# Kernel optimization log

Measured on AMD Instinct MI355X. Metric: run time of the kernel, lower is better.

Reference implementation:

```python
import jax, jax.numpy as jnp
import numpy as np

N_NODES = 100000
N_EDGES = 1600000
IN_CH = 128
HEADS = 4
OUT_CH = 32


def setup_inputs() -> dict:
    key = jax.random.key(0)
    k1, k2, k3, k4 = jax.random.split(key, 4)
    x = jax.random.normal(k1, (N_NODES, IN_CH), dtype=jnp.float32)
    edge_index = jax.random.randint(k2, (2, N_EDGES), 0, N_NODES, dtype=jnp.int64)
    # linear weight stored as [in, heads*out] so projection is x @ W
    W = jax.random.normal(k3, (IN_CH, HEADS * OUT_CH), dtype=jnp.float32) * (1.0 / np.sqrt(IN_CH))
    att = jax.random.normal(k4, (HEADS, OUT_CH), dtype=jnp.float32)
    return {"x": x, "edge_index": edge_index, "W": W, "att": att}


def reference(x, edge_index, W, att):
    N = x.shape[0]
    row, col = edge_index[0], edge_index[1]
    # project and split heads: [N, H, C]
    projected = (x @ W).reshape(N, HEADS, OUT_CH)
    src = projected[row]                      # [E, H, C]
    dst = projected[col]                      # [E, H, C]
    scores = jnp.tanh(src + dst)              # [E, H, C]
    scores = jnp.einsum('ehc,hc->eh', scores, att)  # [E, H]
    # stabilize by global per-head max over edges, then exp
    scores = jnp.exp(scores - jnp.max(scores, axis=0, keepdims=True))
    # scatter-add over destination nodes
    out = jax.ops.segment_sum(src * scores[:, :, None], col, num_segments=N)  # [N, H, C]
    normalizer = jax.ops.segment_sum(scores, col, num_segments=N)             # [N, H]
    out = out / jnp.maximum(normalizer, 1e-12)[:, :, None]
    return out.reshape(N, HEADS * OUT_CH)
```

## Files before the change

kernel.cpp:

```cpp
#include <hip/hip_runtime.h>

#define IN_CH 128
#define HEADS 4
#define OUT_CH 32
#define HC 128
#define SCORE_BLOCKS 4096
#define CHUNK 2048

__device__ __forceinline__ unsigned flip_f32(float x) {
  unsigned u = __float_as_uint(x);
  return (u & 0x80000000u) ? ~u : (u | 0x80000000u);
}
__device__ __forceinline__ float unflip_f32(unsigned k) {
  unsigned u = (k & 0x80000000u) ? (k ^ 0x80000000u) : ~k;
  return __uint_as_float(u);
}
__device__ __forceinline__ float fast_tanh(float x) {
#if __has_builtin(__builtin_amdgcn_exp2f)
  const float t = __builtin_amdgcn_exp2f(x * 2.8853900817779268f);
#else
  const float t = __expf(2.f * x);
#endif
#if __has_builtin(__builtin_amdgcn_rcpf)
  return 1.f - 2.f * __builtin_amdgcn_rcpf(t + 1.f);
#else
  return 1.f - 2.f / (t + 1.f);
#endif
}

__global__ __launch_bounds__(256) void gemm_xW(const float* __restrict__ x,
                                               const float* __restrict__ W,
                                               float* __restrict__ proj, int N,
                                               const int* __restrict__ ecol,
                                               int* __restrict__ hist, int E) {
  __shared__ float xs[128][68];
  __shared__ float ws[128][68];
  const int tid = threadIdx.x;
  const int rowblk = blockIdx.x >> 1;
  const int colblk = blockIdx.x & 1;
  const int row0 = rowblk * 64;
  const int col0 = colblk * 64;

  {
    const int k = tid >> 1;
    const int c0 = (tid & 1) * 32;
    const float4* src = (const float4*)(W + (size_t)k * HC + col0 + c0);
#pragma unroll
    for (int i = 0; i < 8; ++i) *(float4*)&ws[k][c0 + i * 4] = src[i];
  }
  {
    const int r = tid >> 2;
    const int k0 = (tid & 3) * 32;
    const int grow = row0 + r;
    const bool valid = grow < N;
    const float4* src = (const float4*)(x + (size_t)grow * IN_CH + k0);
#pragma unroll
    for (int i = 0; i < 8; ++i) {
      float4 v = valid ? src[i] : make_float4(0.f, 0.f, 0.f, 0.f);
      const int k = k0 + i * 4;
      xs[k][r] = v.x; xs[k + 1][r] = v.y; xs[k + 2][r] = v.z; xs[k + 3][r] = v.w;
    }
  }
  __syncthreads();

  const int cg2 = tid & 15;
  const int rg = tid >> 4;
  float acc[4][4];
#pragma unroll
  for (int r = 0; r < 4; ++r)
#pragma unroll
    for (int c = 0; c < 4; ++c) acc[r][c] = 0.f;

#pragma unroll 8
  for (int k = 0; k < 128; ++k) {
    const float4 a = *(const float4*)&xs[k][rg * 4];
    const float4 b = *(const float4*)&ws[k][cg2 * 4];
    const float xv[4] = {a.x, a.y, a.z, a.w};
    const float wv[4] = {b.x, b.y, b.z, b.w};
#pragma unroll
    for (int r = 0; r < 4; ++r)
#pragma unroll
      for (int c = 0; c < 4; ++c) acc[r][c] += xv[r] * wv[c];
  }

#pragma unroll
  for (int r = 0; r < 4; ++r) {
    const int grow = row0 + rg * 4 + r;
    if (grow < N) {
      *(float4*)(proj + (size_t)grow * HC + col0 + cg2 * 4) =
          make_float4(acc[r][0], acc[r][1], acc[r][2], acc[r][3]);
    }
  }

  if (hist) {
    const int ehb = (E + gridDim.x - 1) / gridDim.x;
    const int estart = blockIdx.x * ehb;
    const int eend = min(estart + ehb, E);
    for (int e = estart + tid; e < eend; e += 256) atomicAdd(&hist[ecol[e]], 1);
  }
}

__device__ __forceinline__ int block_scan_excl(int tsum, int* ls, int tid, int* total) {
  ls[tid] = tsum;
  __syncthreads();
  for (int off = 1; off < 256; off <<= 1) {
    int v = (tid >= off) ? ls[tid - off] : 0;
    __syncthreads();
    ls[tid] += v;
    __syncthreads();
  }
  *total = ls[255];
  return ls[tid] - tsum;
}

__global__ __launch_bounds__(256) void k_scan(const int* __restrict__ hist,
                                              int* __restrict__ sums,
                                              unsigned* __restrict__ flags,
                                              int* __restrict__ starts,
                                              int* __restrict__ cursor,
                                              int nb, int nc) {
  __shared__ int ls[256];
  const int tid = threadIdx.x;
  const int bid = blockIdx.x;
  const int base = bid * CHUNK + tid * 8;
  int h[8];
  int t = 0;
#pragma unroll
  for (int j = 0; j < 8; ++j) {
    const int i = base + j;
    h[j] = (i < nb) ? hist[i] : 0;
    t += h[j];
  }
  int total;
  const int excl = block_scan_excl(t, ls, tid, &total);
  if (tid == 0) {
    __hip_atomic_store(&sums[bid], total, __ATOMIC_RELAXED, __HIP_MEMORY_SCOPE_AGENT);
    __hip_atomic_store(&flags[bid], 1u, __ATOMIC_RELEASE, __HIP_MEMORY_SCOPE_AGENT);
  }
  int my = 0;
  if (tid < bid) {
    while (__hip_atomic_load(&flags[tid], __ATOMIC_ACQUIRE, __HIP_MEMORY_SCOPE_AGENT) == 0u) {}
    my = __hip_atomic_load(&sums[tid], __ATOMIC_RELAXED, __HIP_MEMORY_SCOPE_AGENT);
  }
  __syncthreads();
  ls[tid] = my;
  __syncthreads();
  for (int off = 128; off >= 1; off >>= 1) {
    if (tid < off) ls[tid] += ls[tid + off];
    __syncthreads();
  }
  const int cbase = ls[0];
  int run = cbase + excl;
#pragma unroll
  for (int j = 0; j < 8; ++j) {
    const int i = base + j;
    if (i < nb) { starts[i] = run; cursor[i] = run; run += h[j]; }
  }
  if (bid == nc - 1 && tid == 0) {
    starts[nb] = cbase + total;
    cursor[nb] = cbase + total;
  }
}

__global__ __launch_bounds__(256) void scatter_rc(const int* __restrict__ erow,
                                                  const int* __restrict__ ecol,
                                                  int* __restrict__ cursor,
                                                  int* __restrict__ rc, int E) {
  const int i = blockIdx.x * 256 + threadIdx.x;
  if (i < E) {
    const int p = atomicAdd(&cursor[ecol[i]], 1);
    rc[p] = erow[i] * HC;
  }
}

__global__ __launch_bounds__(256) void fused_apply(const float* __restrict__ proj,
                                                   const int* __restrict__ rc,
                                                   const int* __restrict__ starts,
                                                   const float* __restrict__ att,
                                                   float* __restrict__ out,
                                                   float* __restrict__ den,
                                                   unsigned* __restrict__ headmax_u, int N) {
  __shared__ unsigned blkmax[HEADS];
  const int tid = threadIdx.x;
  if (tid < HEADS) blkmax[tid] = 0u;
  __syncthreads();
  const int lane = tid & 63;
  const int half = lane >> 5;
  const int l = lane & 31;
  const int c0 = l * 4;
  const int head = l >> 3;
  const int n = blockIdx.x * 4 + (tid >> 6);
  float lm = -3.0e38f;

  if (n < N) {
    const float4 a4 = ((const float4*)att)[l];
    float M0 = fabsf(a4.x) + fabsf(a4.y) + fabsf(a4.z) + fabsf(a4.w);
    M0 += __shfl_xor(M0, 4, 64);
    M0 += __shfl_xor(M0, 2, 64);
    M0 += __shfl_xor(M0, 1, 64);
    const float4 d4 = *(const float4*)(proj + (size_t)n * HC + c0);
    const int beg = __builtin_amdgcn_readfirstlane(starts[n]);
    const int end = __builtin_amdgcn_readfirstlane(starts[n + 1]);

    float ax = 0.f, ay = 0.f, az = 0.f, aw = 0.f, dsum = 0.f;
    int i = beg;
    for (; i + 8 <= end; i += 8) {
      const int r0 = rc[i + half];
      const int r1 = rc[i + 2 + half];
      const int r2 = rc[i + 4 + half];
      const int r3 = rc[i + 6 + half];
      const float4 s0 = *(const float4*)(proj + r0 + c0);
      const float4 s1 = *(const float4*)(proj + r1 + c0);
      const float4 s2 = *(const float4*)(proj + r2 + c0);
      const float4 s3 = *(const float4*)(proj + r3 + c0);
      float p0 = fast_tanh(s0.x + d4.x) * a4.x + fast_tanh(s0.y + d4.y) * a4.y
               + fast_tanh(s0.z + d4.z) * a4.z + fast_tanh(s0.w + d4.w) * a4.w;
      float p1 = fast_tanh(s1.x + d4.x) * a4.x + fast_tanh(s1.y + d4.y) * a4.y
               + fast_tanh(s1.z + d4.z) * a4.z + fast_tanh(s1.w + d4.w) * a4.w;
      float p2 = fast_tanh(s2.x + d4.x) * a4.x + fast_tanh(s2.y + d4.y) * a4.y
               + fast_tanh(s2.z + d4.z) * a4.z + fast_tanh(s2.w + d4.w) * a4.w;
      float p3 = fast_tanh(s3.x + d4.x) * a4.x + fast_tanh(s3.y + d4.y) * a4.y
               + fast_tanh(s3.z + d4.z) * a4.z + fast_tanh(s3.w + d4.w) * a4.w;
      p0 += __shfl_xor(p0, 4, 64);  p1 += __shfl_xor(p1, 4, 64);
      p2 += __shfl_xor(p2, 4, 64);  p3 += __shfl_xor(p3, 4, 64);
      p0 += __shfl_xor(p0, 2, 64);  p1 += __shfl_xor(p1, 2, 64);
      p2 += __shfl_xor(p2, 2, 64);  p3 += __shfl_xor(p3, 2, 64);
      p0 += __shfl_xor(p0, 1, 64);  p1 += __shfl_xor(p1, 1, 64);
      p2 += __shfl_xor(p2, 1, 64);  p3 += __shfl_xor(p3, 1, 64);
      lm = fmaxf(lm, fmaxf(fmaxf(p0, p1), fmaxf(p2, p3)));
      const float e0 = __expf(p0 - M0);
      const float e1 = __expf(p1 - M0);
      const float e2 = __expf(p2 - M0);
      const float e3 = __expf(p3 - M0);
      ax += s0.x * e0 + s1.x * e1 + s2.x * e2 + s3.x * e3;
      ay += s0.y * e0 + s1.y * e1 + s2.y * e2 + s3.y * e3;
      az += s0.z * e0 + s1.z * e1 + s2.z * e2 + s3.z * e3;
      aw += s0.w * e0 + s1.w * e1 + s2.w * e2 + s3.w * e3;
      dsum += (e0 + e1) + (e2 + e3);
    }
    if (i + 4 <= end) {
      const int r0 = rc[i + half];
      const int r1 = rc[i + 2 + half];
      const float4 s0 = *(const float4*)(proj + r0 + c0);
      const float4 s1 = *(const float4*)(proj + r1 + c0);
      float p0 = fast_tanh(s0.x + d4.x) * a4.x + fast_tanh(s0.y + d4.y) * a4.y
               + fast_tanh(s0.z + d4.z) * a4.z + fast_tanh(s0.w + d4.w) * a4.w;
      float p1 = fast_tanh(s1.x + d4.x) * a4.x + fast_tanh(s1.y + d4.y) * a4.y
               + fast_tanh(s1.z + d4.z) * a4.z + fast_tanh(s1.w + d4.w) * a4.w;
      p0 += __shfl_xor(p0, 4, 64);  p1 += __shfl_xor(p1, 4, 64);
      p0 += __shfl_xor(p0, 2, 64);  p1 += __shfl_xor(p1, 2, 64);
      p0 += __shfl_xor(p0, 1, 64);  p1 += __shfl_xor(p1, 1, 64);
      lm = fmaxf(lm, fmaxf(p0, p1));
      const float e0 = __expf(p0 - M0);
      const float e1 = __expf(p1 - M0);
      ax += s0.x * e0 + s1.x * e1;
      ay += s0.y * e0 + s1.y * e1;
      az += s0.z * e0 + s1.z * e1;
      aw += s0.w * e0 + s1.w * e1;
      dsum += e0 + e1;
      i += 4;
    }
    for (; i < end; i += 2) {
      const int idx = i + half;
      const bool valid = idx < end;
      const int row = rc[valid ? idx : i];
      const float4 s4 = *(const float4*)(proj + row + c0);
      float p = fast_tanh(s4.x + d4.x) * a4.x
              + fast_tanh(s4.y + d4.y) * a4.y
              + fast_tanh(s4.z + d4.z) * a4.z
              + fast_tanh(s4.w + d4.w) * a4.w;
      p += __shfl_xor(p, 4, 64);
      p += __shfl_xor(p, 2, 64);
      p += __shfl_xor(p, 1, 64);
      if (!valid) p = -3.0e38f;
      lm = fmaxf(lm, p);
      const float e = __expf(p - M0);
      ax += s4.x * e; ay += s4.y * e; az += s4.z * e; aw += s4.w * e;
      dsum += e;
    }
    dsum += __shfl_xor(dsum, 32, 64);
    ax += __shfl_xor(ax, 32, 64);
    ay += __shfl_xor(ay, 32, 64);
    az += __shfl_xor(az, 32, 64);
    aw += __shfl_xor(aw, 32, 64);
    lm = fmaxf(lm, __shfl_xor(lm, 32, 64));
    if (half == 0) {
      const float inv = 1.f / fmaxf(dsum, 1e-38f);
      *(float4*)(out + (size_t)n * HC + c0) =
          make_float4(ax * inv, ay * inv, az * inv, aw * inv);
      if ((l & 7) == 0) den[n * HEADS + head] = dsum;
      if ((l & 7) == 0) atomicMax(&blkmax[head], flip_f32(lm));
    }
  }
  __syncthreads();
  if (tid < HEADS) {
    const unsigned v = blkmax[tid];
    if (v > headmax_u[tid]) atomicMax(&headmax_u[tid], v);
  }
}

__global__ __launch_bounds__(256) void fix_clamp(float* __restrict__ out,
                                                 const float* __restrict__ den,
                                                 const unsigned* __restrict__ headmax_u,
                                                 const float* __restrict__ att, int N) {
  const int t = blockIdx.x * 256 + threadIdx.x;
  if (t >= N * HEADS) return;
  const int n = t >> 2;
  const int h = t & 3;
  float M0 = 0.f;
#pragma unroll
  for (int c = 0; c < OUT_CH; ++c) M0 += fabsf(att[h * OUT_CH + c]);
  const float Mt = unflip_f32(headmax_u[h]);
  const float f = den[t] * __expf(M0 - Mt);
  if (f < 1e-12f) {
    const float s = f * 1e12f;
    float4* p = (float4*)(out + (size_t)n * HC + h * OUT_CH);
#pragma unroll
    for (int j = 0; j < 8; ++j) {
      float4 v = p[j];
      v.x *= s; v.y *= s; v.z *= s; v.w *= s;
      p[j] = v;
    }
  }
}

__global__ __launch_bounds__(256) void reduce_corr(const unsigned* __restrict__ blockmax,
                                                   const float* __restrict__ att,
                                                   float* __restrict__ corr, int nblk) {
  __shared__ unsigned sm[HEADS];
  const int tid = threadIdx.x;
  if (tid < HEADS) sm[tid] = 0u;
  __syncthreads();
  const int h = tid & 3;
  unsigned k = 0u;
  for (int i = tid >> 2; i < nblk; i += 64) k = max(k, blockmax[i * HEADS + h]);
  atomicMax(&sm[h], k);
  __syncthreads();
  if (tid < HEADS) {
    const float Mt = unflip_f32(sm[tid]);
    float M0 = 0.f;
#pragma unroll
    for (int c = 0; c < OUT_CH; ++c) M0 += fabsf(att[tid * OUT_CH + c]);
    corr[tid] = __expf(M0 - Mt);
    corr[4 + tid] = Mt;
  }
}

__global__ __launch_bounds__(256) void score_max(const float* __restrict__ proj,
                                                 const int* __restrict__ erow,
                                                 const int* __restrict__ ecol,
                                                 const float* __restrict__ att,
                                                 unsigned* __restrict__ blockmax, int E) {
  __shared__ unsigned blkmax[HEADS];
  const int tid = threadIdx.x;
  if (tid < HEADS) blkmax[tid] = 0u;
  __syncthreads();
  const int lane = tid & 63;
  const int wid = tid >> 6;
  const float a0 = att[lane];
  const float a1 = att[lane + 64];
  float lmA = -3.0e38f, lmB = -3.0e38f;
  const int stride = SCORE_BLOCKS * 16;

  for (int base = (blockIdx.x * 4 + wid) * 4; base < E; base += stride) {
    const int bu = __builtin_amdgcn_readfirstlane(base);
    const int lim = min(bu + 4, E);
    for (int e = bu; e < lim; ++e) {
      const int r0 = erow[e], c0 = ecol[e];
      const float* ps = proj + (size_t)r0 * HC;
      const float* pd = proj + (size_t)c0 * HC;
      float pA = fast_tanh(ps[lane] + pd[lane]) * a0;
      float pB = fast_tanh(ps[lane + 64] + pd[lane + 64]) * a1;
#pragma unroll
      for (int m = 16; m >= 1; m >>= 1) {
        pA += __shfl_xor(pA, m, 64);
        pB += __shfl_xor(pB, m, 64);
      }
      lmA = fmaxf(lmA, pA);
      lmB = fmaxf(lmB, pB);
    }
  }
  if ((lane & 31) == 0) {
    const int hh = lane >> 5;
    atomicMax(&blkmax[hh], flip_f32(lmA));
    atomicMax(&blkmax[hh + 2], flip_f32(lmB));
  }
  __syncthreads();
  if (tid < HEADS) blockmax[blockIdx.x * HEADS + tid] = blkmax[tid];
}

__global__ __launch_bounds__(256) void edge_apply_fb(const float* __restrict__ proj,
                                                     const int* __restrict__ erow,
                                                     const int* __restrict__ ecol,
                                                     const float* __restrict__ att,
                                                     const float* __restrict__ headmax,
                                                     float* __restrict__ out,
                                                     float* __restrict__ norm, int E) {
  const int tid = threadIdx.x;
  const int e = blockIdx.x * 2 + (tid >> 7);
  if (e >= E) return;
  const int ch = tid & 127;
  const int h = ch >> 5;
  const float M = headmax[h];
  const int row = erow[e];
  const int col = ecol[e];
  const float sv = proj[(size_t)row * HC + ch];
  const float dv = proj[(size_t)col * HC + ch];
  float p = fast_tanh(sv + dv) * att[ch];
#pragma unroll
  for (int m = 16; m >= 1; m >>= 1) p += __shfl_xor(p, m, 64);
  const float w = __expf(p - M);
  unsafeAtomicAdd(&out[(size_t)col * HC + ch], sv * w);
  if ((ch & 31) == 0) unsafeAtomicAdd(&norm[(size_t)col * HEADS + h], w);
}

__global__ __launch_bounds__(256) void finalize_fb(float* __restrict__ out,
                                                   const float* __restrict__ norm, int N) {
  const int idx = blockIdx.x * blockDim.x + threadIdx.x;
  const int total = N * (HC / 4);
  if (idx >= total) return;
  const int base = idx * 4;
  const int node = base >> 7;
  const int h = (base >> 5) & 3;
  const float inv = 1.f / fmaxf(norm[node * HEADS + h], 1e-12f);
  float4 v = ((float4*)out)[idx];
  v.x *= inv; v.y *= inv; v.z *= inv; v.w *= inv;
  ((float4*)out)[idx] = v;
}

extern "C" void kernel_launch(void* const* d_in, const int* in_sizes, int n_in,
                              void* d_out, int out_size, void* d_ws, size_t ws_size,
                              hipStream_t stream) {
  const float* x    = (const float*)d_in[0];
  const int*   eidx = (const int*)d_in[1];
  const float* W    = (const float*)d_in[2];
  const float* att  = (const float*)d_in[3];
  float* out = (float*)d_out;

  const int N = in_sizes[0] / IN_CH;
  const int E = in_sizes[1] / 2;
  const int nb = N;
  const int nc = (nb + CHUNK - 1) / CHUNK;
  const int ngemm = ((N + 63) / 64) * 2;

  char* p = (char*)d_ws;
  float* proj = (float*)p;  p += (size_t)N * HC * 4;
  int* rc = (int*)p;        p += (((size_t)E * 4 + 15) & ~15ull);
  float* den = (float*)p;   p += (((size_t)N * HEADS * 4 + 15) & ~15ull);
  int* hist = (int*)p;      p += (((size_t)(nb + 4 + 256) * 4 + 15) & ~15ull);
  int* starts = (int*)p;    p += (((size_t)(nb + 1) * 4 + 15) & ~15ull);
  int* cursor = (int*)p;    p += (((size_t)(nb + 1) * 4 + 15) & ~15ull);
  int* sums = (int*)p;      p += 1024;
  unsigned* headmax_u = (unsigned*)(hist + nb);
  unsigned* flags = (unsigned*)(hist + nb + 4);
  const size_t need_full = (size_t)(p - (char*)d_ws);
  const bool full = (ws_size >= need_full) && (nc <= 256);

  if (full) {
    hipMemsetAsync(hist, 0, (size_t)(nb + 4 + 256) * sizeof(int), stream);
    gemm_xW<<<ngemm, 256, 0, stream>>>(x, W, proj, N, eidx + E, hist, E);
    k_scan<<<nc, 256, 0, stream>>>(hist, sums, flags, starts, cursor, nb, nc);
    scatter_rc<<<(E + 255) / 256, 256, 0, stream>>>(eidx, eidx + E, cursor, rc, E);
    fused_apply<<<(N + 3) / 4, 256, 0, stream>>>(proj, rc, starts, att, out, den,
                                                 headmax_u, N);
    fix_clamp<<<(N * HEADS + 255) / 256, 256, 0, stream>>>(out, den, headmax_u, att, N);
  } else {
    gemm_xW<<<ngemm, 256, 0, stream>>>(x, W, proj, N, nullptr, nullptr, 0);
    unsigned* bm = (unsigned*)(proj + (size_t)N * HC);
    float* cr = (float*)(bm + SCORE_BLOCKS * HEADS);
    float* norm = cr + 8;
    hipMemsetAsync(out, 0, (size_t)out_size * sizeof(float), stream);
    hipMemsetAsync(norm, 0, (size_t)N * HEADS * sizeof(float), stream);
    score_max<<<SCORE_BLOCKS, 256, 0, stream>>>(proj, eidx, eidx + E, att, bm, E);
    reduce_corr<<<1, 256, 0, stream>>>(bm, att, cr, SCORE_BLOCKS);
    edge_apply_fb<<<(E + 1) / 2, 256, 0, stream>>>(proj, eidx, eidx + E, att, cr + 4, out, norm, E);
    finalize_fb<<<(N * (HC / 4) + 255) / 256, 256, 0, stream>>>(out, norm, N);
  }
}
```

Baseline: 454.0 us.

## Replace global-atomic CSR scatter with two-pass bucketed counting sort

Swaps the single scatter kernel, which did one global atomicAdd per edge on a per-node cursor and wrote to random positions, for a two-pass bucket sort. The first pass groups edges into buckets of 512 destination nodes using shared-memory atomics and one global atomic per bucket per block. The second pass places each bucket's edges into CSR order with shared-memory atomics, so global writes stay local. This adds an 8-byte-per-edge intermediate buffer and an extra kernel launch, and rc order within a node is still non-deterministic.

New measurement: 425.2 us. 1.07x faster.

```diff
diff --git a/kernel.cpp b/kernel.cpp
--- a/kernel.cpp
+++ b/kernel.cpp
@@ -6,6 +6,8 @@
 #define HC 128
 #define SCORE_BLOCKS 4096
 #define CHUNK 2048
+#define BW_SHIFT 9
+#define BW (1 << BW_SHIFT)
 
 __device__ __forceinline__ unsigned flip_f32(float x) {
   unsigned u = __float_as_uint(x);
@@ -117,7 +119,6 @@
                                               int* __restrict__ sums,
                                               unsigned* __restrict__ flags,
                                               int* __restrict__ starts,
-                                              int* __restrict__ cursor,
                                               int nb, int nc) {
   __shared__ int ls[256];
   const int tid = threadIdx.x;
@@ -154,22 +155,65 @@
 #pragma unroll
   for (int j = 0; j < 8; ++j) {
     const int i = base + j;
-    if (i < nb) { starts[i] = run; cursor[i] = run; run += h[j]; }
-  }
-  if (bid == nc - 1 && tid == 0) {
-    starts[nb] = cbase + total;
-    cursor[nb] = cbase + total;
-  }
-}
-
-__global__ __launch_bounds__(256) void scatter_rc(const int* __restrict__ erow,
-                                                  const int* __restrict__ ecol,
-                                                  int* __restrict__ cursor,
-                                                  int* __restrict__ rc, int E) {
-  const int i = blockIdx.x * 256 + threadIdx.x;
-  if (i < E) {
-    const int p = atomicAdd(&cursor[ecol[i]], 1);
-    rc[p] = erow[i] * HC;
+    if (i < nb) { starts[i] = run; run += h[j]; }
+  }
+  if (bid == nc - 1 && tid == 0) starts[nb] = cbase + total;
+}
+
+__global__ __launch_bounds__(256) void bucket_split(const int* __restrict__ erow,
+                                                    const int* __restrict__ ecol,
+                                                    const int* __restrict__ starts,
+                                                    int* __restrict__ bcnt,
+                                                    int2* __restrict__ aux,
+                                                    int E, int NB) {
+  __shared__ int cnt[1024];
+  __shared__ int base[1024];
+  const int tid = threadIdx.x;
+  for (int b = tid; b < NB; b += 256) cnt[b] = 0;
+  __syncthreads();
+  const int e0 = blockIdx.x * 2048;
+  int rows[8], cols[8], loc[8];
+#pragma unroll
+  for (int j = 0; j < 8; ++j) {
+    const int e = e0 + j * 256 + tid;
+    if (e < E) {
+      cols[j] = ecol[e];
+      rows[j] = erow[e];
+      loc[j] = atomicAdd(&cnt[cols[j] >> BW_SHIFT], 1);
+    } else {
+      loc[j] = -1;
+    }
+  }
+  __syncthreads();
+  for (int b = tid; b < NB; b += 256) {
+    const int c = cnt[b];
+    base[b] = (c ? atomicAdd(&bcnt[b], c) : 0) + starts[b << BW_SHIFT];
+  }
+  __syncthreads();
+#pragma unroll
+  for (int j = 0; j < 8; ++j) {
+    if (loc[j] >= 0) {
+      const int b = cols[j] >> BW_SHIFT;
+      aux[base[b] + loc[j]] = make_int2(rows[j] * HC, cols[j]);
+    }
+  }
+}
+
+__global__ __launch_bounds__(256) void bucket_place(const int2* __restrict__ aux,
+                                                    const int* __restrict__ starts,
+                                                    int* __restrict__ rc, int N) {
+  __shared__ int lcnt[BW];
+  const int tid = threadIdx.x;
+  const int n0 = blockIdx.x << BW_SHIFT;
+  const int n1 = min(n0 + BW, N);
+  for (int i = tid; i < BW; i += 256) lcnt[i] = 0;
+  __syncthreads();
+  const int e0 = starts[n0];
+  const int e1 = starts[n1];
+  for (int i = e0 + tid; i < e1; i += 256) {
+    const int2 pr = aux[i];
+    const int r = atomicAdd(&lcnt[pr.y & (BW - 1)], 1);
+    rc[starts[pr.y] + r] = pr.x;
   }
 }
 
@@ -441,26 +485,30 @@
   const int E = in_sizes[1] / 2;
   const int nb = N;
   const int nc = (nb + CHUNK - 1) / CHUNK;
+  const int NB = (N + BW - 1) >> BW_SHIFT;
   const int ngemm = ((N + 63) / 64) * 2;
 
   char* p = (char*)d_ws;
   float* proj = (float*)p;  p += (size_t)N * HC * 4;
   int* rc = (int*)p;        p += (((size_t)E * 4 + 15) & ~15ull);
   float* den = (float*)p;   p += (((size_t)N * HEADS * 4 + 15) & ~15ull);
-  int* hist = (int*)p;      p += (((size_t)(nb + 4 + 256) * 4 + 15) & ~15ull);
+  int* hist = (int*)p;      p += (((size_t)(nb + 4 + 256 + NB) * 4 + 15) & ~15ull);
   int* starts = (int*)p;    p += (((size_t)(nb + 1) * 4 + 15) & ~15ull);
-  int* cursor = (int*)p;    p += (((size_t)(nb + 1) * 4 + 15) & ~15ull);
+  int2* aux = (int2*)p;     p += (((size_t)E * 8 + 15) & ~15ull);
   int* sums = (int*)p;      p += 1024;
   unsigned* headmax_u = (unsigned*)(hist + nb);
   unsigned* flags = (unsigned*)(hist + nb + 4);
+  int* bcnt = hist + nb + 4 + 256;
   const size_t need_full = (size_t)(p - (char*)d_ws);
-  const bool full = (ws_size >= need_full) && (nc <= 256);
+  const bool full = (ws_size >= need_full) && (nc <= 256) && (NB <= 1024);
 
   if (full) {
-    hipMemsetAsync(hist, 0, (size_t)(nb + 4 + 256) * sizeof(int), stream);
+    hipMemsetAsync(hist, 0, (size_t)(nb + 4 + 256 + NB) * sizeof(int), stream);
     gemm_xW<<<ngemm, 256, 0, stream>>>(x, W, proj, N, eidx + E, hist, E);
-    k_scan<<<nc, 256, 0, stream>>>(hist, sums, flags, starts, cursor, nb, nc);
-    scatter_rc<<<(E + 255) / 256, 256, 0, stream>>>(eidx, eidx + E, cursor, rc, E);
+    k_scan<<<nc, 256, 0, stream>>>(hist, sums, flags, starts, nb, nc);
+    bucket_split<<<(E + 2047) / 2048, 256, 0, stream>>>(eidx, eidx + E, starts,
+                                                        bcnt, aux, E, NB);
+    bucket_place<<<NB, 256, 0, stream>>>(aux, starts, rc, N);
     fused_apply<<<(N + 3) / 4, 256, 0, stream>>>(proj, rc, starts, att, out, den,
                                                  headmax_u, N);
     fix_clamp<<<(N * HEADS + 255) / 256, 256, 0, stream>>>(out, den, headmax_u, att, N);
```
